# Optimization experiments

Hardware: AMD Instinct MI355X
Metric: run time of the kernel (lower is better)

The kernel has to match this reference:

```python
import jax, jax.numpy as jnp
import numpy as np

D_MODEL, D_EDGE, D_STRUCT = 128, 64, 8
N, E, B = 50000, 800000, 1

def _lin(key, din, dout):
    kw, kb = jax.random.split(key)
    s = 1.0 / np.sqrt(din)
    return (jax.random.uniform(kw, (din, dout), jnp.float32, -s, s),
            jax.random.uniform(kb, (dout,), jnp.float32, -s, s))

def setup_inputs() -> dict:
    key = jax.random.key(0)
    ks = jax.random.split(key, 16)
    H = jax.random.normal(ks[0], (B, N, D_MODEL), jnp.float32)
    xyz = jax.random.normal(ks[1], (B, N, 3), jnp.float32)
    edge_index = jax.random.randint(ks[2], (2, E), 0, N, jnp.int64)
    edge_struct = jax.random.normal(ks[3], (E, D_STRUCT), jnp.float32)
    edge_rest_lengths = jax.random.uniform(ks[4], (E,), jnp.float32)
    We1, be1 = _lin(ks[5], 2 * D_MODEL + 2 + D_STRUCT, D_EDGE)
    We2, be2 = _lin(ks[6], D_EDGE, D_EDGE)
    Wg1, bg1 = _lin(ks[7], 2 + D_STRUCT, 32)
    Wg2, bg2 = _lin(ks[8], 32, 1)
    Wn1, bn1 = _lin(ks[9], D_MODEL + D_EDGE, 2 * D_MODEL)
    Wn2, bn2 = _lin(ks[10], 2 * D_MODEL, D_MODEL)
    ln_g = jnp.ones((D_MODEL,), jnp.float32)
    ln_b = jnp.zeros((D_MODEL,), jnp.float32)
    return dict(H=H, xyz=xyz, edge_index=edge_index, edge_struct=edge_struct,
                edge_rest_lengths=edge_rest_lengths,
                We1=We1, be1=be1, We2=We2, be2=be2,
                Wg1=Wg1, bg1=bg1, Wg2=Wg2, bg2=bg2,
                Wn1=Wn1, bn1=bn1, Wn2=Wn2, bn2=bn2,
                ln_g=ln_g, ln_b=ln_b)

def reference(H, xyz, edge_index, edge_struct, edge_rest_lengths,
              We1, be1, We2, be2, Wg1, bg1, Wg2, bg2,
              Wn1, bn1, Wn2, bn2, ln_g, ln_b):
    Bn, Nn, d = H.shape
    i, j = edge_index[0], edge_index[1]
    # edge geometry
    diff = xyz[:, i, :] - xyz[:, j, :]                      # (B,E,3)
    dist2 = jnp.sum(diff * diff, axis=-1, keepdims=True)    # (B,E,1)
    dist = jnp.sqrt(dist2 + 1e-9)
    rest = edge_rest_lengths.reshape(1, -1, 1)
    delta = (dist - rest) / (rest + 1e-9)
    struct = jnp.broadcast_to(edge_struct[None], (Bn, edge_struct.shape[0], edge_struct.shape[1]))
    # edge message MLP
    Hi, Hj = H[:, i, :], H[:, j, :]
    e_in = jnp.concatenate([Hi, Hj, dist2, delta, struct], axis=-1)  # (B,E,2d+2+ds)
    e = jax.nn.silu(e_in @ We1 + be1)
    e_msg = jax.nn.silu(e @ We2 + be2)                       # (B,E,d_edge)
    # gate
    g_in = jnp.concatenate([dist2, delta, struct], axis=-1)
    g = jax.nn.sigmoid(jax.nn.silu(g_in @ Wg1 + bg1) @ Wg2 + bg2)  # (B,E,1)
    e_msg = e_msg * g
    # scatter-add aggregate to destination node i
    agg = jnp.zeros((Bn, Nn, e_msg.shape[-1]), H.dtype).at[:, i, :].add(e_msg)
    # node MLP (dropout is identity at eval) + residual + LayerNorm
    n_in = jnp.concatenate([H, agg], axis=-1)
    upd = jax.nn.silu(n_in @ Wn1 + bn1) @ Wn2 + bn2
    x = H + upd
    mu = jnp.mean(x, axis=-1, keepdims=True)
    var = jnp.mean((x - mu) ** 2, axis=-1, keepdims=True)
    return (x - mu) / jnp.sqrt(var + 1e-5) * ln_g + ln_b
```

## Files before the change

### kernel.cpp

```cpp
#include <hip/hip_runtime.h>
#include <stdint.h>

#define N_NODES 50000
#define N_EDGES 800000
#define NODE_TILES 782

#define SE   72
#define SW2  72
#define SPQ  136
#define SN1  216
#define SN2  280
#define ATS  40
#define MSTR 72

#define EC_GRID 962
#define EC_CHUNK 13

#define SCAN_B 98

typedef short bf16x8 __attribute__((ext_vector_type(8)));
typedef short short4v __attribute__((ext_vector_type(4)));
typedef unsigned short ushort8 __attribute__((ext_vector_type(8)));
typedef float f32x4  __attribute__((ext_vector_type(4)));

static __device__ __forceinline__ unsigned short f2bf(float f) {
  unsigned int x = __float_as_uint(f);
  unsigned int r = (x + 0x7fffu + ((x >> 16) & 1u)) >> 16;
  return (unsigned short)r;
}
static __device__ __forceinline__ float bf2f(unsigned short u) {
  return __uint_as_float(((unsigned int)u) << 16);
}
static __device__ __forceinline__ float silu_f(float x) {
  return x * __builtin_amdgcn_rcpf(1.0f + __expf(-x));
}
static __device__ __forceinline__ float sigmoid_f(float x) {
  return __builtin_amdgcn_rcpf(1.0f + __expf(-x));
}
static __device__ __forceinline__ unsigned int cvt_pk_bf16(float lo, float hi) {
  unsigned int r;
  asm("v_cvt_pk_bf16_f32 %0, %1, %2" : "=v"(r) : "v"(lo), "v"(hi));
  return r;
}
static __device__ __forceinline__ bf16x8 pack8(float4 u, float4 v) {
  bf16x8 w;
  w[0] = (short)f2bf(u.x); w[1] = (short)f2bf(u.y);
  w[2] = (short)f2bf(u.z); w[3] = (short)f2bf(u.w);
  w[4] = (short)f2bf(v.x); w[5] = (short)f2bf(v.y);
  w[6] = (short)f2bf(v.z); w[7] = (short)f2bf(v.w);
  return w;
}

__global__ void prep_hist(
    const int* __restrict__ eidx,
    const float* __restrict__ We1, const float* __restrict__ be1,
    const float* __restrict__ We2,
    const float* __restrict__ Wn1, const float* __restrict__ Wn2,
    unsigned short* __restrict__ WpqT, unsigned short* __restrict__ We2T,
    unsigned short* __restrict__ Wn1T, unsigned short* __restrict__ Wn2T,
    unsigned short* __restrict__ WrT,
    int* __restrict__ cnt)
{
  const int gid = blockIdx.x * 256 + threadIdx.x;
  const int gsz = gridDim.x * 256;
  for (int i = gid; i < 128 * SPQ; i += gsz) {
    int n = i / SPQ, k = i % SPQ;
    unsigned short v = 0;
    if (k < 128) v = (n < 64) ? f2bf(We1[k * 64 + n]) : f2bf(We1[(128 + k) * 64 + (n - 64)]);
    WpqT[i] = v;
  }
  for (int i = gid; i < 64 * SW2; i += gsz) {
    int n = i / SW2, k = i % SW2;
    We2T[i] = (k < 64) ? f2bf(We2[k * 64 + n]) : (unsigned short)0;
  }
  for (int i = gid; i < 256 * SN1; i += gsz) {
    int n = i / SN1, k = i % SN1;
    Wn1T[i] = (k < 192) ? f2bf(Wn1[k * 256 + n]) : (unsigned short)0;
  }
  for (int i = gid; i < 128 * SN2; i += gsz) {
    int n = i / SN2, k = i % SN2;
    Wn2T[i] = (k < 256) ? f2bf(Wn2[k * 128 + n]) : (unsigned short)0;
  }
  for (int i = gid; i < 64 * 32; i += gsz) {
    int n = i >> 5, k = i & 31;
    float v = 0.f;
    if (k < 2)       v = We1[256 * 64 + n];
    else if (k < 4)  v = We1[257 * 64 + n];
    else if (k < 12) v = We1[(258 + (k - 4)) * 64 + n];
    else if (k == 12) v = be1[n];
    else if (k == 13) { float w = We1[256 * 64 + n]; v = w - bf2f(f2bf(w)); }
    else if (k == 14) { float w = We1[257 * 64 + n]; v = w - bf2f(f2bf(w)); }
    else if (k == 15) { float w = be1[n];            v = w - bf2f(f2bf(w)); }
    WrT[i] = (k < 16) ? f2bf(v) : (unsigned short)0;
  }
  if (gid < N_EDGES) atomicAdd(&cnt[eidx[gid]], 1);
}

__global__ __launch_bounds__(512) void scan_local(
    const int* __restrict__ cnt, int* __restrict__ rowptr,
    int* __restrict__ bsum)
{
  __shared__ int wsum[8], woff[8];
  const int t = threadIdx.x;
  const int idx = blockIdx.x * 512 + t;
  const int lane = t & 63, wid = t >> 6;
  int c = (idx < N_NODES) ? cnt[idx] : 0;
  int v = c;
  #pragma unroll
  for (int o = 1; o < 64; o <<= 1) {
    int u = __shfl_up(v, o);
    if (lane >= o) v += u;
  }
  if (lane == 63) wsum[wid] = v;
  __syncthreads();
  if (t == 0) {
    int a = 0;
    #pragma unroll
    for (int w = 0; w < 8; ++w) { woff[w] = a; a += wsum[w]; }
    bsum[blockIdx.x] = a;
  }
  __syncthreads();
  if (idx < N_NODES) rowptr[idx] = woff[wid] + (v - c);
}

__global__ __launch_bounds__(128) void scan_mid(
    const int* __restrict__ bsum, int* __restrict__ boff)
{
  __shared__ int ws[2];
  const int t = threadIdx.x;
  const int lane = t & 63, wid = t >> 6;
  int c = (t < SCAN_B) ? bsum[t] : 0;
  int v = c;
  #pragma unroll
  for (int o = 1; o < 64; o <<= 1) {
    int u = __shfl_up(v, o);
    if (lane >= o) v += u;
  }
  if (lane == 63) ws[wid] = v;
  __syncthreads();
  int add = (wid == 1) ? ws[0] : 0;
  if (t < SCAN_B) boff[t] = add + (v - c);
}

__global__ __launch_bounds__(512) void scan_add(
    const int* __restrict__ rowptr, const int* __restrict__ boff,
    int* __restrict__ cursor)
{
  const int idx = blockIdx.x * 512 + threadIdx.x;
  if (idx < N_NODES) cursor[idx] = rowptr[idx] + boff[blockIdx.x];
}

__global__ void fill_reorder(
    const int* __restrict__ eidx, const float* __restrict__ xyz,
    const float* __restrict__ estruct, const float* __restrict__ erest,
    int* __restrict__ cursor,
    const float* __restrict__ Wg1, const float* __restrict__ bg1,
    const float* __restrict__ Wg2, const float* __restrict__ bg2,
    float4* __restrict__ metaA, unsigned short* __restrict__ sst,
    int* __restrict__ in_s)
{
  int e = blockIdx.x * 256 + threadIdx.x;
  if (e >= N_EDGES) return;
  int i = eidx[e], j = eidx[N_EDGES + e];
  float dx = xyz[i * 3 + 0] - xyz[j * 3 + 0];
  float dy = xyz[i * 3 + 1] - xyz[j * 3 + 1];
  float dz = xyz[i * 3 + 2] - xyz[j * 3 + 2];
  float d2 = dx * dx + dy * dy + dz * dz;
  float dist = sqrtf(d2 + 1e-9f);
  float rest = erest[e];
  float dl = (dist - rest) / (rest + 1e-9f);
  float4 s0 = *(const float4*)&estruct[e * 8];
  float4 s1 = *(const float4*)&estruct[e * 8 + 4];
  float st[8] = {s0.x, s0.y, s0.z, s0.w, s1.x, s1.y, s1.z, s1.w};
  float gsum = 0.f;
  #pragma unroll
  for (int h = 0; h < 32; ++h) {
    float a = bg1[h] + d2 * Wg1[0 * 32 + h] + dl * Wg1[1 * 32 + h];
    #pragma unroll
    for (int c = 0; c < 8; ++c) a += st[c] * Wg1[(2 + c) * 32 + h];
    gsum += silu_f(a) * Wg2[h];
  }
  float g = sigmoid_f(gsum + bg2[0]);

  int pos = atomicAdd(&cursor[i], 1);
  metaA[pos] = make_float4(d2, dl, g, __int_as_float(j));
  ushort8 w;
  #pragma unroll
  for (int c = 0; c < 8; ++c) w[c] = f2bf(st[c]);
  *(ushort8*)&sst[(long)pos * 8] = w;
  in_s[pos] = i;
}

__global__ __launch_bounds__(256, 2) void pq_kernel(
    const float* __restrict__ H, const unsigned short* __restrict__ WpqT,
    unsigned short* __restrict__ P, unsigned short* __restrict__ Q,
    unsigned short* __restrict__ Hbf)
{
  __shared__ unsigned short As[64 * SPQ];
  __shared__ unsigned short Ws[128 * SPQ];

  const int tid  = threadIdx.x;
  const int lane = tid & 63;
  const int wv   = tid >> 6;
  const int lr   = lane & 15;
  const int lq   = lane >> 4;
  const int m0   = wv * 16;
  const int n0   = blockIdx.x * 64;

  for (int i = tid * 8; i < 128 * SPQ; i += 256 * 8)
    *(bf16x8*)&Ws[i] = *(const bf16x8*)&WpqT[i];
  {
    int le = tid >> 2, q = tid & 3;
    int node = n0 + le; if (node >= N_NODES) node = N_NODES - 1;
    const float* src = H + (long)node * 128 + q * 32;
    unsigned short* dst = &As[le * SPQ + q * 32];
    #pragma unroll
    for (int c = 0; c < 32; c += 8) {
      float4 u = *(const float4*)(src + c);
      float4 v = *(const float4*)(src + c + 4);
      *(bf16x8*)(dst + c) = pack8(u, v);
    }
  }
  __syncthreads();

  for (int idx = tid * 8; idx < 64 * 128; idx += 256 * 8) {
    int row = idx >> 7, col = idx & 127;
    *(bf16x8*)&Hbf[((long)n0 + row) * 128 + col] = *(const bf16x8*)&As[row * SPQ + col];
  }

  f32x4 zero4 = {0.f, 0.f, 0.f, 0.f};
  f32x4 acc[8];
  #pragma unroll
  for (int f = 0; f < 8; ++f) acc[f] = zero4;
  #pragma unroll
  for (int s = 0; s < 4; ++s) {
    int kb = s * 32 + lq * 8;
    bf16x8 a = *(const bf16x8*)&As[(m0 + lr) * SPQ + kb];
    #pragma unroll
    for (int f = 0; f < 8; ++f) {
      bf16x8 b = *(const bf16x8*)&Ws[(f * 16 + lr) * SPQ + kb];
      acc[f] = __builtin_amdgcn_mfma_f32_16x16x32_bf16(a, b, acc[f], 0, 0, 0);
    }
  }
  #pragma unroll
  for (int f = 0; f < 8; ++f) {
    #pragma unroll
    for (int r = 0; r < 4; ++r) {
      int node = n0 + m0 + lq * 4 + r;
      if (node < N_NODES) {
        if (f < 4) P[(long)node * 64 + f * 16 + lr] = f2bf(acc[f][r]);
        else       Q[(long)node * 64 + (f - 4) * 16 + lr] = f2bf(acc[f][r]);
      }
    }
  }
}

__global__ __launch_bounds__(256, 4) void edge_compute(
    const unsigned short* __restrict__ P, const unsigned short* __restrict__ Q,
    const int* __restrict__ in_s,
    const float4* __restrict__ metaA, const unsigned short* __restrict__ sst,
    const unsigned short* __restrict__ We2T, const float* __restrict__ be2,
    const unsigned short* __restrict__ WrT,
    float* __restrict__ agg)
{
  __shared__ unsigned short W2s[64 * SW2];
  __shared__ unsigned short Es [4 * 16 * SE];
  __shared__ unsigned short At [4 * 16 * ATS];
  __shared__ unsigned short Ms [4 * 16 * MSTR];

  const int tid  = threadIdx.x;
  const int lane = tid & 63;
  const int wv   = tid >> 6;
  const int lr   = lane & 15;
  const int lq   = lane >> 4;

  for (int i = tid * 8; i < 64 * SW2; i += 256 * 8)
    *(bf16x8*)&W2s[i] = *(const bf16x8*)&We2T[i];

  unsigned short* Es_w = &Es[wv * 16 * SE];
  unsigned short* At_w = &At[wv * 16 * ATS];
  unsigned short* Ms_w = &Ms[wv * 16 * MSTR];

  if (lane < 16) {
    ushort8 z;
    #pragma unroll
    for (int c = 0; c < 8; ++c) z[c] = 0;
    *(ushort8*)&At_w[lane * ATS + 16] = z;
    *(ushort8*)&At_w[lane * ATS + 24] = z;
  }

  bf16x8 aWr[4];
  float bias2[4][4];
  #pragma unroll
  for (int f = 0; f < 4; ++f) {
    aWr[f] = *(const bf16x8*)&WrT[(f * 16 + lr) * 32 + lq * 8];
    #pragma unroll
    for (int r = 0; r < 4; ++r) bias2[f][r] = be2[f * 16 + lq * 4 + r];
  }
  __syncthreads();

  const int n_tiles = N_EDGES / 16;
  const int wid = blockIdx.x * 4 + wv;
  const int t0 = wid * EC_CHUNK;
  const int t1 = (t0 + EC_CHUNK < n_tiles) ? (t0 + EC_CHUNK) : n_tiles;
  if (t0 >= n_tiles) return;

  f32x4 zero4 = {0.f, 0.f, 0.f, 0.f};
  int   cur_node   = in_s[t0 * 16];
  float acc        = 0.f;
  bool  use_atomic = true;

  for (int tile = t0; tile < t1; ++tile) {
    const int s0 = tile * 16;

    float4 mm = metaA[s0 + lr];
    int   inode = in_s[s0 + lr];
    int   jnode = __float_as_int(mm.w);
    float g     = mm.z;

    if (lane < 16) {
      ushort8 sv = *(const ushort8*)&sst[(long)(s0 + lane) * 8];
      float d2 = mm.x, dl = mm.y;
      unsigned short d2h = f2bf(d2);
      unsigned short d2l = f2bf(d2 - bf2f(d2h));
      unsigned short dlh = f2bf(dl);
      unsigned short dll = f2bf(dl - bf2f(dlh));
      ushort8 w0, w1;
      w0[0] = d2h;   w0[1] = d2l;   w0[2] = dlh;   w0[3] = dll;
      w0[4] = sv[0]; w0[5] = sv[1]; w0[6] = sv[2]; w0[7] = sv[3];
      w1[0] = sv[4]; w1[1] = sv[5]; w1[2] = sv[6]; w1[3] = sv[7];
      w1[4] = 0x3F80u; w1[5] = d2h; w1[6] = dlh;  w1[7] = 0x3F80u;
      *(ushort8*)&At_w[lane * ATS]     = w0;
      *(ushort8*)&At_w[lane * ATS + 8] = w1;
    }

    bf16x8 bA = *(const bf16x8*)&At_w[lr * ATS + lq * 8];
    f32x4 acc1[4];
    #pragma unroll
    for (int f = 0; f < 4; ++f)
      acc1[f] = __builtin_amdgcn_mfma_f32_16x16x32_bf16(aWr[f], bA, zero4, 0, 0, 0);

    const unsigned short* Pb = P + (long)inode * 64;
    const unsigned short* Qb = Q + (long)jnode * 64;
    #pragma unroll
    for (int f = 0; f < 4; ++f) {
      short4v pv = *(const short4v*)&Pb[f * 16 + lq * 4];
      short4v qv = *(const short4v*)&Qb[f * 16 + lq * 4];
      float v0 = silu_f(bf2f((unsigned short)pv[0]) + bf2f((unsigned short)qv[0]) + acc1[f][0]);
      float v1 = silu_f(bf2f((unsigned short)pv[1]) + bf2f((unsigned short)qv[1]) + acc1[f][1]);
      float v2 = silu_f(bf2f((unsigned short)pv[2]) + bf2f((unsigned short)qv[2]) + acc1[f][2]);
      float v3 = silu_f(bf2f((unsigned short)pv[3]) + bf2f((unsigned short)qv[3]) + acc1[f][3]);
      uint2 w;
      w.x = cvt_pk_bf16(v0, v1);
      w.y = cvt_pk_bf16(v2, v3);
      *(uint2*)&Es_w[lr * SE + f * 16 + lq * 4] = w;
    }

    f32x4 acc2[4];
    #pragma unroll
    for (int f = 0; f < 4; ++f) acc2[f] = zero4;
    #pragma unroll
    for (int s = 0; s < 2; ++s) {
      int kb = s * 32 + lq * 8;
      bf16x8 bE = *(const bf16x8*)&Es_w[lr * SE + kb];
      #pragma unroll
      for (int f = 0; f < 4; ++f) {
        bf16x8 aW = *(const bf16x8*)&W2s[(f * 16 + lr) * SW2 + kb];
        acc2[f] = __builtin_amdgcn_mfma_f32_16x16x32_bf16(aW, bE, acc2[f], 0, 0, 0);
      }
    }

    #pragma unroll
    for (int f = 0; f < 4; ++f) {
      float o0 = silu_f(acc2[f][0] + bias2[f][0]) * g;
      float o1 = silu_f(acc2[f][1] + bias2[f][1]) * g;
      float o2 = silu_f(acc2[f][2] + bias2[f][2]) * g;
      float o3 = silu_f(acc2[f][3] + bias2[f][3]) * g;
      uint2 w;
      w.x = cvt_pk_bf16(o0, o1);
      w.y = cvt_pk_bf16(o2, o3);
      *(uint2*)&Ms_w[lr * MSTR + f * 16 + lq * 4] = w;
    }

    #pragma unroll
    for (int e = 0; e < 16; ++e) {
      int ie = __builtin_amdgcn_readlane(inode, e);
      if (ie != cur_node) {
        if (use_atomic) atomicAdd(&agg[(long)cur_node * 64 + lane], acc);
        else            agg[(long)cur_node * 64 + lane] = acc;
        use_atomic = false;
        cur_node = ie;
        acc = 0.f;
      }
      acc += bf2f(Ms_w[e * MSTR + lane]);
    }
  }
  atomicAdd(&agg[(long)cur_node * 64 + lane], acc);
}

__global__ __launch_bounds__(256, 2) void h1_kernel(
    const unsigned short* __restrict__ Hbf, const float* __restrict__ agg,
    const unsigned short* __restrict__ Wn1T, const float* __restrict__ bn1,
    unsigned short* __restrict__ h1)
{
  __shared__ unsigned short Wl[128 * SN1];

  const int tid  = threadIdx.x;
  const int lane = tid & 63;
  const int wv   = tid >> 6;
  const int lr   = lane & 15;
  const int lq   = lane >> 4;
  const int m0   = wv * 16;
  const int p    = blockIdx.x & 1;

  for (int i = tid * 8; i < 128 * SN1; i += 256 * 8)
    *(bf16x8*)&Wl[i] = *(const bf16x8*)&Wn1T[p * 128 * SN1 + i];
  __syncthreads();

  f32x4 zero4 = {0.f, 0.f, 0.f, 0.f};
  for (int t = blockIdx.x >> 1; t < NODE_TILES; t += 256) {
    const int n0 = t * 64;
    int rowa = n0 + m0 + lr;
    int rowc = rowa < N_NODES ? rowa : N_NODES - 1;

    f32x4 acc1[8];
    #pragma unroll
    for (int f = 0; f < 8; ++f) acc1[f] = zero4;
    #pragma unroll
    for (int s = 0; s < 6; ++s) {
      int kb = s * 32 + lq * 8;
      bf16x8 a;
      if (s < 4) {
        a = *(const bf16x8*)&Hbf[(long)rowa * 128 + kb];
      } else {
        const float* pp = agg + (long)rowc * 64 + (kb - 128);
        float4 u = *(const float4*)pp;
        float4 v = *(const float4*)(pp + 4);
        a = pack8(u, v);
      }
      #pragma unroll
      for (int f = 0; f < 8; ++f) {
        bf16x8 b = *(const bf16x8*)&Wl[(f * 16 + lr) * SN1 + kb];
        acc1[f] = __builtin_amdgcn_mfma_f32_16x16x32_bf16(a, b, acc1[f], 0, 0, 0);
      }
    }
    #pragma unroll
    for (int f = 0; f < 8; ++f) {
      int col = p * 128 + f * 16 + lr;
      float bias = bn1[col];
      #pragma unroll
      for (int r = 0; r < 4; ++r) {
        int node = n0 + m0 + lq * 4 + r;
        h1[(long)node * 256 + col] = f2bf(silu_f(acc1[f][r] + bias));
      }
    }
  }
}

__global__ __launch_bounds__(256, 2) void out_kernel(
    const float* __restrict__ H, const unsigned short* __restrict__ h1,
    const unsigned short* __restrict__ Wn2T, const float* __restrict__ bn2,
    const float* __restrict__ ln_g, const float* __restrict__ ln_b,
    float* __restrict__ out)
{
  __shared__ unsigned short Wl[128 * SN2];

  const int tid  = threadIdx.x;
  const int lane = tid & 63;
  const int wv   = tid >> 6;
  const int lr   = lane & 15;
  const int lq   = lane >> 4;
  const int m0   = wv * 16;

  for (int i = tid * 8; i < 128 * SN2; i += 256 * 8)
    *(bf16x8*)&Wl[i] = *(const bf16x8*)&Wn2T[i];
  __syncthreads();

  f32x4 zero4 = {0.f, 0.f, 0.f, 0.f};
  for (int t = blockIdx.x; t < NODE_TILES; t += 512) {
    const int n0 = t * 64;
    int rowa = n0 + m0 + lr;

    f32x4 acc2[8];
    #pragma unroll
    for (int f = 0; f < 8; ++f) acc2[f] = zero4;
    #pragma unroll
    for (int s = 0; s < 8; ++s) {
      int kb = s * 32 + lq * 8;
      bf16x8 a = *(const bf16x8*)&h1[(long)rowa * 256 + kb];
      #pragma unroll
      for (int f = 0; f < 8; ++f) {
        bf16x8 b = *(const bf16x8*)&Wl[(f * 16 + lr) * SN2 + kb];
        acc2[f] = __builtin_amdgcn_mfma_f32_16x16x32_bf16(a, b, acc2[f], 0, 0, 0);
      }
    }

    #pragma unroll
    for (int r = 0; r < 4; ++r) {
      int node = n0 + m0 + lq * 4 + r;
      int nc = node < N_NODES ? node : N_NODES - 1;
      float x[8];
      float sum = 0.f, sumsq = 0.f;
      #pragma unroll
      for (int f = 0; f < 8; ++f) {
        int n = f * 16 + lr;
        float u = acc2[f][r] + bn2[n];
        float xv = H[(long)nc * 128 + n] + u;
        x[f] = xv;
        sum += xv;
        sumsq += xv * xv;
      }
      #pragma unroll
      for (int o = 1; o < 16; o <<= 1) {
        sum   += __shfl_xor(sum, o);
        sumsq += __shfl_xor(sumsq, o);
      }
      float mu  = sum * (1.f / 128.f);
      float var = sumsq * (1.f / 128.f) - mu * mu;
      float rstd = rsqrtf(var + 1e-5f);
      if (node < N_NODES) {
        #pragma unroll
        for (int f = 0; f < 8; ++f) {
          int n = f * 16 + lr;
          out[(long)node * 128 + n] = (x[f] - mu) * rstd * ln_g[n] + ln_b[n];
        }
      }
    }
  }
}

extern "C" void kernel_launch(void* const* d_in, const int* in_sizes, int n_in,
                              void* d_out, int out_size, void* d_ws, size_t ws_size,
                              hipStream_t stream) {
  const float* H       = (const float*)d_in[0];
  const float* xyz     = (const float*)d_in[1];
  const int*   eidx    = (const int*)d_in[2];
  const float* estruct = (const float*)d_in[3];
  const float* erest   = (const float*)d_in[4];
  const float* We1     = (const float*)d_in[5];
  const float* be1     = (const float*)d_in[6];
  const float* We2     = (const float*)d_in[7];
  const float* be2     = (const float*)d_in[8];
  const float* Wg1     = (const float*)d_in[9];
  const float* bg1     = (const float*)d_in[10];
  const float* Wg2     = (const float*)d_in[11];
  const float* bg2     = (const float*)d_in[12];
  const float* Wn1     = (const float*)d_in[13];
  const float* bn1     = (const float*)d_in[14];
  const float* Wn2     = (const float*)d_in[15];
  const float* bn2     = (const float*)d_in[16];
  const float* ln_g    = (const float*)d_in[17];
  const float* ln_b    = (const float*)d_in[18];

  char* ws = (char*)d_ws;
  float*          agg    = (float*)(ws + 0);
  unsigned short* Hbf    = (unsigned short*)(ws + 12812288);
  float4*         metaA  = (float4*)(ws + 25624576);
  unsigned short* sst    = (unsigned short*)(ws + 38424576);
  int*            in_s   = (int*)(ws + 51224576);
  unsigned short* P      = (unsigned short*)(ws + 54424576);
  unsigned short* Qm     = (unsigned short*)(ws + 60824576);
  int*            cnt    = (int*)(ws + 67224576);
  int*            rowptr = (int*)(ws + 67424768);
  int*            cursor = (int*)(ws + 67624960);
  unsigned short* WpqT   = (unsigned short*)(ws + 67825152);
  unsigned short* We2T   = (unsigned short*)(ws + 67859968);
  unsigned short* Wn1T   = (unsigned short*)(ws + 67871232);
  unsigned short* Wn2T   = (unsigned short*)(ws + 67981824);
  unsigned short* WrT    = (unsigned short*)(ws + 68053504);
  int*            bsum   = (int*)(ws + 68057600);
  int*            boff   = (int*)(ws + 68058112);
  unsigned short* h1     = (unsigned short*)(ws + 68058624);
  float* out = (float*)d_out;

  hipMemsetAsync(cnt, 0, (size_t)N_NODES * sizeof(int), stream);
  hipMemsetAsync(agg, 0, (size_t)50048 * 64 * sizeof(float), stream);

  hipLaunchKernelGGL(prep_hist, dim3(3125), dim3(256), 0, stream,
                     eidx, We1, be1, We2, Wn1, Wn2, WpqT, We2T, Wn1T, Wn2T, WrT, cnt);
  hipLaunchKernelGGL(scan_local, dim3(SCAN_B), dim3(512), 0, stream,
                     cnt, rowptr, bsum);
  hipLaunchKernelGGL(scan_mid, dim3(1), dim3(128), 0, stream,
                     bsum, boff);
  hipLaunchKernelGGL(scan_add, dim3(SCAN_B), dim3(512), 0, stream,
                     rowptr, boff, cursor);
  hipLaunchKernelGGL(fill_reorder, dim3(3125), dim3(256), 0, stream,
                     eidx, xyz, estruct, erest, cursor,
                     Wg1, bg1, Wg2, bg2, metaA, sst, in_s);
  hipLaunchKernelGGL(pq_kernel, dim3(NODE_TILES), dim3(256), 0, stream,
                     H, WpqT, P, Qm, Hbf);
  hipLaunchKernelGGL(edge_compute, dim3(EC_GRID), dim3(256), 0, stream,
                     P, Qm, in_s, metaA, sst, We2T, be2, WrT, agg);
  hipLaunchKernelGGL(h1_kernel, dim3(512), dim3(256), 0, stream,
                     Hbf, agg, Wn1T, bn1, h1);
  hipLaunchKernelGGL(out_kernel, dim3(512), dim3(256), 0, stream,
                     H, h1, Wn2T, bn2, ln_g, ln_b, out);
}
```

Before: 389.7 us.

## Pack per-edge metadata into one 32-byte record and fold agg zeroing into scan

The separate metaA, sst and in_s arrays are replaced by a single 32-byte per-edge record. It holds the pre-split bf16 hi/lo pairs for d2 and delta, the bf16 struct features, the gate value, and i/j packed as 16-bit indices. This cuts bytes written by fill_reorder and read by edge_compute, and moves the bf16 splitting out of the edge loop. The agg memset is folded into scan_add, and pq_kernel becomes a grid-stride loop over 512 blocks so the weight tile is loaded into LDS fewer times. Packing node indices into 16 bits only works because N is below 65536, and the agg zeroing in scan_add uses strided per-thread stores.

```diff
diff --git a/kernel.cpp b/kernel.cpp
--- a/kernel.cpp
+++ b/kernel.cpp
@@ -144,10 +144,16 @@
 
 __global__ __launch_bounds__(512) void scan_add(
     const int* __restrict__ rowptr, const int* __restrict__ boff,
-    int* __restrict__ cursor)
+    int* __restrict__ cursor, float4* __restrict__ agg)
 {
   const int idx = blockIdx.x * 512 + threadIdx.x;
   if (idx < N_NODES) cursor[idx] = rowptr[idx] + boff[blockIdx.x];
+  if (idx < 50048) {
+    float4 z = make_float4(0.f, 0.f, 0.f, 0.f);
+    float4* p = agg + (long)idx * 16;
+    #pragma unroll
+    for (int k = 0; k < 16; ++k) p[k] = z;
+  }
 }
 
 __global__ void fill_reorder(
@@ -156,8 +162,7 @@
     int* __restrict__ cursor,
     const float* __restrict__ Wg1, const float* __restrict__ bg1,
     const float* __restrict__ Wg2, const float* __restrict__ bg2,
-    float4* __restrict__ metaA, unsigned short* __restrict__ sst,
-    int* __restrict__ in_s)
+    unsigned short* __restrict__ rec)
 {
   int e = blockIdx.x * 256 + threadIdx.x;
   if (e >= N_EDGES) return;
@@ -182,13 +187,24 @@
   }
   float g = sigmoid_f(gsum + bg2[0]);
 
+  unsigned short d2h = f2bf(d2);
+  unsigned short d2l = f2bf(d2 - bf2f(d2h));
+  unsigned short dlh = f2bf(dl);
+  unsigned short dll = f2bf(dl - bf2f(dlh));
+
+  ushort8 w0;
+  w0[0] = d2h; w0[1] = d2l; w0[2] = dlh; w0[3] = dll;
+  w0[4] = f2bf(st[0]); w0[5] = f2bf(st[1]); w0[6] = f2bf(st[2]); w0[7] = f2bf(st[3]);
+  uint4 w1;
+  w1.x = (unsigned int)f2bf(st[4]) | ((unsigned int)f2bf(st[5]) << 16);
+  w1.y = (unsigned int)f2bf(st[6]) | ((unsigned int)f2bf(st[7]) << 16);
+  w1.z = __float_as_uint(g);
+  w1.w = (unsigned int)i | ((unsigned int)j << 16);
+
   int pos = atomicAdd(&cursor[i], 1);
-  metaA[pos] = make_float4(d2, dl, g, __int_as_float(j));
-  ushort8 w;
-  #pragma unroll
-  for (int c = 0; c < 8; ++c) w[c] = f2bf(st[c]);
-  *(ushort8*)&sst[(long)pos * 8] = w;
-  in_s[pos] = i;
+  unsigned short* dst = rec + (long)pos * 16;
+  *(ushort8*)dst = w0;
+  *(uint4*)(dst + 8) = w1;
 }
 
 __global__ __launch_bounds__(256, 2) void pq_kernel(
@@ -205,51 +221,55 @@
   const int lr   = lane & 15;
   const int lq   = lane >> 4;
   const int m0   = wv * 16;
-  const int n0   = blockIdx.x * 64;
 
   for (int i = tid * 8; i < 128 * SPQ; i += 256 * 8)
     *(bf16x8*)&Ws[i] = *(const bf16x8*)&WpqT[i];
-  {
-    int le = tid >> 2, q = tid & 3;
-    int node = n0 + le; if (node >= N_NODES) node = N_NODES - 1;
-    const float* src = H + (long)node * 128 + q * 32;
-    unsigned short* dst = &As[le * SPQ + q * 32];
-    #pragma unroll
-    for (int c = 0; c < 32; c += 8) {
-      float4 u = *(const float4*)(src + c);
-      float4 v = *(const float4*)(src + c + 4);
-      *(bf16x8*)(dst + c) = pack8(u, v);
-    }
-  }
-  __syncthreads();
-
-  for (int idx = tid * 8; idx < 64 * 128; idx += 256 * 8) {
-    int row = idx >> 7, col = idx & 127;
-    *(bf16x8*)&Hbf[((long)n0 + row) * 128 + col] = *(const bf16x8*)&As[row * SPQ + col];
-  }
 
   f32x4 zero4 = {0.f, 0.f, 0.f, 0.f};
-  f32x4 acc[8];
-  #pragma unroll
-  for (int f = 0; f < 8; ++f) acc[f] = zero4;
-  #pragma unroll
-  for (int s = 0; s < 4; ++s) {
-    int kb = s * 32 + lq * 8;
-    bf16x8 a = *(const bf16x8*)&As[(m0 + lr) * SPQ + kb];
+  for (int t = blockIdx.x; t < NODE_TILES; t += 512) {
+    const int n0 = t * 64;
+    __syncthreads();
+    {
+      int le = tid >> 2, q = tid & 3;
+      int node = n0 + le; if (node >= N_NODES) node = N_NODES - 1;
+      const float* src = H + (long)node * 128 + q * 32;
+      unsigned short* dst = &As[le * SPQ + q * 32];
+      #pragma unroll
+      for (int c = 0; c < 32; c += 8) {
+        float4 u = *(const float4*)(src + c);
+        float4 v = *(const float4*)(src + c + 4);
+        *(bf16x8*)(dst + c) = pack8(u, v);
+      }
+    }
+    __syncthreads();
+
+    for (int idx = tid * 8; idx < 64 * 128; idx += 256 * 8) {
+      int row = idx >> 7, col = idx & 127;
+      *(bf16x8*)&Hbf[((long)n0 + row) * 128 + col] = *(const bf16x8*)&As[row * SPQ + col];
+    }
+
+    f32x4 acc[8];
+    #pragma unroll
+    for (int f = 0; f < 8; ++f) acc[f] = zero4;
+    #pragma unroll
+    for (int s = 0; s < 4; ++s) {
+      int kb = s * 32 + lq * 8;
+      bf16x8 a = *(const bf16x8*)&As[(m0 + lr) * SPQ + kb];
+      #pragma unroll
+      for (int f = 0; f < 8; ++f) {
+        bf16x8 b = *(const bf16x8*)&Ws[(f * 16 + lr) * SPQ + kb];
+        acc[f] = __builtin_amdgcn_mfma_f32_16x16x32_bf16(a, b, acc[f], 0, 0, 0);
+      }
+    }
     #pragma unroll
     for (int f = 0; f < 8; ++f) {
-      bf16x8 b = *(const bf16x8*)&Ws[(f * 16 + lr) * SPQ + kb];
-      acc[f] = __builtin_amdgcn_mfma_f32_16x16x32_bf16(a, b, acc[f], 0, 0, 0);
-    }
-  }
-  #pragma unroll
-  for (int f = 0; f < 8; ++f) {
-    #pragma unroll
-    for (int r = 0; r < 4; ++r) {
-      int node = n0 + m0 + lq * 4 + r;
-      if (node < N_NODES) {
-        if (f < 4) P[(long)node * 64 + f * 16 + lr] = f2bf(acc[f][r]);
-        else       Q[(long)node * 64 + (f - 4) * 16 + lr] = f2bf(acc[f][r]);
+      #pragma unroll
+      for (int r = 0; r < 4; ++r) {
+        int node = n0 + m0 + lq * 4 + r;
+        if (node < N_NODES) {
+          if (f < 4) P[(long)node * 64 + f * 16 + lr] = f2bf(acc[f][r]);
+          else       Q[(long)node * 64 + (f - 4) * 16 + lr] = f2bf(acc[f][r]);
+        }
       }
     }
   }
@@ -257,8 +277,7 @@
 
 __global__ __launch_bounds__(256, 4) void edge_compute(
     const unsigned short* __restrict__ P, const unsigned short* __restrict__ Q,
-    const int* __restrict__ in_s,
-    const float4* __restrict__ metaA, const unsigned short* __restrict__ sst,
+    const unsigned short* __restrict__ rec,
     const unsigned short* __restrict__ We2T, const float* __restrict__ be2,
     const unsigned short* __restrict__ WrT,
     float* __restrict__ agg)
@@ -306,31 +325,33 @@
   if (t0 >= n_tiles) return;
 
   f32x4 zero4 = {0.f, 0.f, 0.f, 0.f};
-  int   cur_node   = in_s[t0 * 16];
+  int   cur_node;
+  {
+    int ij0 = *(const int*)(rec + (long)t0 * 16 * 16 + 14);
+    cur_node = ij0 & 0xffff;
+  }
   float acc        = 0.f;
   bool  use_atomic = true;
 
   for (int tile = t0; tile < t1; ++tile) {
     const int s0 = tile * 16;
 
-    float4 mm = metaA[s0 + lr];
-    int   inode = in_s[s0 + lr];
-    int   jnode = __float_as_int(mm.w);
-    float g     = mm.z;
+    const unsigned short* rp = rec + (long)(s0 + lr) * 16;
+    ushort8 ra = *(const ushort8*)rp;
+    uint4   rb = *(const uint4*)(rp + 8);
+    float g     = __uint_as_float(rb.z);
+    int   inode = rb.w & 0xffff;
+    int   jnode = (rb.w >> 16) & 0xffff;
 
     if (lane < 16) {
-      ushort8 sv = *(const ushort8*)&sst[(long)(s0 + lane) * 8];
-      float d2 = mm.x, dl = mm.y;
-      unsigned short d2h = f2bf(d2);
-      unsigned short d2l = f2bf(d2 - bf2f(d2h));
-      unsigned short dlh = f2bf(dl);
-      unsigned short dll = f2bf(dl - bf2f(dlh));
-      ushort8 w0, w1;
-      w0[0] = d2h;   w0[1] = d2l;   w0[2] = dlh;   w0[3] = dll;
-      w0[4] = sv[0]; w0[5] = sv[1]; w0[6] = sv[2]; w0[7] = sv[3];
-      w1[0] = sv[4]; w1[1] = sv[5]; w1[2] = sv[6]; w1[3] = sv[7];
-      w1[4] = 0x3F80u; w1[5] = d2h; w1[6] = dlh;  w1[7] = 0x3F80u;
-      *(ushort8*)&At_w[lane * ATS]     = w0;
+      ushort8 w1;
+      w1[0] = (unsigned short)(rb.x & 0xffff);
+      w1[1] = (unsigned short)(rb.x >> 16);
+      w1[2] = (unsigned short)(rb.y & 0xffff);
+      w1[3] = (unsigned short)(rb.y >> 16);
+      w1[4] = 0x3F80u; w1[5] = (unsigned short)ra[0];
+      w1[6] = (unsigned short)ra[2]; w1[7] = 0x3F80u;
+      *(ushort8*)&At_w[lane * ATS]     = ra;
       *(ushort8*)&At_w[lane * ATS + 8] = w1;
     }
 
@@ -555,26 +576,23 @@
   char* ws = (char*)d_ws;
   float*          agg    = (float*)(ws + 0);
   unsigned short* Hbf    = (unsigned short*)(ws + 12812288);
-  float4*         metaA  = (float4*)(ws + 25624576);
-  unsigned short* sst    = (unsigned short*)(ws + 38424576);
-  int*            in_s   = (int*)(ws + 51224576);
-  unsigned short* P      = (unsigned short*)(ws + 54424576);
-  unsigned short* Qm     = (unsigned short*)(ws + 60824576);
-  int*            cnt    = (int*)(ws + 67224576);
-  int*            rowptr = (int*)(ws + 67424768);
-  int*            cursor = (int*)(ws + 67624960);
-  unsigned short* WpqT   = (unsigned short*)(ws + 67825152);
-  unsigned short* We2T   = (unsigned short*)(ws + 67859968);
-  unsigned short* Wn1T   = (unsigned short*)(ws + 67871232);
-  unsigned short* Wn2T   = (unsigned short*)(ws + 67981824);
-  unsigned short* WrT    = (unsigned short*)(ws + 68053504);
-  int*            bsum   = (int*)(ws + 68057600);
-  int*            boff   = (int*)(ws + 68058112);
-  unsigned short* h1     = (unsigned short*)(ws + 68058624);
+  unsigned short* rec    = (unsigned short*)(ws + 25624576);
+  unsigned short* P      = (unsigned short*)(ws + 51224576);
+  unsigned short* Qm     = (unsigned short*)(ws + 57624576);
+  int*            cnt    = (int*)(ws + 64024576);
+  int*            rowptr = (int*)(ws + 64224768);
+  int*            cursor = (int*)(ws + 64424960);
+  unsigned short* WpqT   = (unsigned short*)(ws + 64625152);
+  unsigned short* We2T   = (unsigned short*)(ws + 64659968);
+  unsigned short* Wn1T   = (unsigned short*)(ws + 64669184);
+  unsigned short* Wn2T   = (unsigned short*)(ws + 64779776);
+  unsigned short* WrT    = (unsigned short*)(ws + 64851456);
+  int*            bsum   = (int*)(ws + 64855552);
+  int*            boff   = (int*)(ws + 64856064);
+  unsigned short* h1     = (unsigned short*)(ws + 64856576);
   float* out = (float*)d_out;
 
   hipMemsetAsync(cnt, 0, (size_t)N_NODES * sizeof(int), stream);
-  hipMemsetAsync(agg, 0, (size_t)50048 * 64 * sizeof(float), stream);
 
   hipLaunchKernelGGL(prep_hist, dim3(3125), dim3(256), 0, stream,
                      eidx, We1, be1, We2, Wn1, Wn2, WpqT, We2T, Wn1T, Wn2T, WrT, cnt);
@@ -583,14 +601,14 @@
   hipLaunchKernelGGL(scan_mid, dim3(1), dim3(128), 0, stream,
                      bsum, boff);
   hipLaunchKernelGGL(scan_add, dim3(SCAN_B), dim3(512), 0, stream,
-                     rowptr, boff, cursor);
+                     rowptr, boff, cursor, (float4*)agg);
   hipLaunchKernelGGL(fill_reorder, dim3(3125), dim3(256), 0, stream,
                      eidx, xyz, estruct, erest, cursor,
-                     Wg1, bg1, Wg2, bg2, metaA, sst, in_s);
-  hipLaunchKernelGGL(pq_kernel, dim3(NODE_TILES), dim3(256), 0, stream,
+                     Wg1, bg1, Wg2, bg2, rec);
+  hipLaunchKernelGGL(pq_kernel, dim3(512), dim3(256), 0, stream,
                      H, WpqT, P, Qm, Hbf);
   hipLaunchKernelGGL(edge_compute, dim3(EC_GRID), dim3(256), 0, stream,
-                     P, Qm, in_s, metaA, sst, We2T, be2, WrT, agg);
+                     P, Qm, rec, We2T, be2, WrT, agg);
   hipLaunchKernelGGL(h1_kernel, dim3(512), dim3(256), 0, stream,
                      Hbf, agg, Wn1T, bn1, h1);
   hipLaunchKernelGGL(out_kernel, dim3(512), dim3(256), 0, stream,
```

Measured after the change: 368.2 us. -5.5%, faster.
